# Kernel optimization log

Measured on AMD Instinct MI355X. Metric: run time of the kernel, lower is better.

## Reference

```python
import jax, jax.numpy as jnp
import numpy as np

N = 4096      # tokens per modality
DIM = 514     # input feature dim
OUT = 256     # out_dim (per-head width, head=1)
NC = 2        # num_classes
LN_EPS = 1e-5


def setup_inputs() -> dict:
    key = jax.random.key(0)
    ks = jax.random.split(key, 12)
    def nrm(k, shape, s=0.02):
        return jax.random.normal(k, shape, dtype=jnp.float32) * s
    return {
        "t1": jax.random.normal(ks[0], (N, DIM), dtype=jnp.float32),
        "t2": jax.random.normal(ks[1], (N, DIM), dtype=jnp.float32),
        "t1c": jax.random.normal(ks[2], (N, DIM), dtype=jnp.float32),
        "Wqkv1": nrm(ks[3], (DIM, 3 * OUT)), "bqkv1": jnp.zeros((3 * OUT,), jnp.float32),
        "Wqkv2": nrm(ks[4], (DIM, 3 * OUT)), "bqkv2": jnp.zeros((3 * OUT,), jnp.float32),
        "Wqkv3": nrm(ks[5], (DIM, 3 * OUT)), "bqkv3": jnp.zeros((3 * OUT,), jnp.float32),
        "Wo1": nrm(ks[6], (2 * OUT, DIM)), "bo1": jnp.zeros((DIM,), jnp.float32),
        "Wo2": nrm(ks[7], (2 * OUT, DIM)), "bo2": jnp.zeros((DIM,), jnp.float32),
        "Wo3": nrm(ks[8], (2 * OUT, DIM)), "bo3": jnp.zeros((DIM,), jnp.float32),
        "ln_g": jnp.ones((3 * DIM,), jnp.float32),
        "ln_b": jnp.zeros((3 * DIM,), jnp.float32),
        "Wh": nrm(ks[9], (3 * DIM, NC)), "bh": jnp.zeros((NC,), jnp.float32),
    }


def _forward(t1, t2, t1c, Wqkv1, bqkv1, Wqkv2, bqkv2, Wqkv3, bqkv3,
             Wo1, bo1, Wo2, bo2, Wo3, bo3, ln_g, ln_b, Wh, bh):
    # QKV projections (head=1 so no head reshape needed)
    q1, k1, v1 = jnp.split(t1 @ Wqkv1 + bqkv1, 3, axis=-1)   # each [n, OUT]
    q2, k2, v2 = jnp.split(t2 @ Wqkv2 + bqkv2, 3, axis=-1)
    q3, k3, v3 = jnp.split(t1c @ Wqkv3 + bqkv3, 3, axis=-1)

    # Six cross-attention instances batched into one group dim g=6.
    # Order: out12, out13, out21, out23, out31, out32  (q_x attends to k_y/v_y)
    qs = jnp.stack([q2, q3, q1, q3, q1, q2])                  # [6, n, OUT]
    ks_ = jnp.stack([k1, k1, k2, k2, k3, k3])
    vs = jnp.stack([v1, v1, v2, v2, v3, v3])
    # NOTE: original code applies NO 1/sqrt(d) scale
    attn = jax.nn.softmax(jnp.einsum('gid,gjd->gij', qs, ks_), axis=-1)
    outs = jnp.einsum('gij,gjd->gid', attn, vs)               # [6, n, OUT]
    out12, out13, out21, out23, out31, out32 = outs

    # residual add with duplicated keys, then per-modality output proj + residual
    t1r = jnp.concatenate([out21, out31], -1) + jnp.concatenate([k1, k1], -1)
    t2r = jnp.concatenate([out12, out32], -1) + jnp.concatenate([k2, k2], -1)
    t3r = jnp.concatenate([out13, out23], -1) + jnp.concatenate([k3, k3], -1)
    a1 = t1r @ Wo1 + bo1 + t1                                 # [n, DIM]
    a2 = t2r @ Wo2 + bo2 + t2
    a3 = t3r @ Wo3 + bo3 + t1c

    atten = jnp.concatenate([a1, a2, a3], -1)                 # [n, 3*DIM]
    mu = jnp.mean(atten, axis=-1, keepdims=True)
    var = jnp.var(atten, axis=-1, keepdims=True)
    normed = (atten - mu) * jax.lax.rsqrt(var + LN_EPS) * ln_g + ln_b
    out = normed @ Wh + bh                                    # [n, NC]
    feat = atten[None]                                        # [1, n, 3*DIM]
    return out, feat


def reference(t1, t2, t1c, Wqkv1, bqkv1, Wqkv2, bqkv2, Wqkv3, bqkv3,
              Wo1, bo1, Wo2, bo2, Wo3, bo3, ln_g, ln_b, Wh, bh):
    return _forward(t1, t2, t1c, Wqkv1, bqkv1, Wqkv2, bqkv2, Wqkv3, bqkv3,
                    Wo1, bo1, Wo2, bo2, Wo3, bo3, ln_g, ln_b, Wh, bh)
```

## Files before the change

kernel.cpp:

```cpp
#include <hip/hip_runtime.h>
#include <hip/hip_bf16.h>

typedef unsigned short u16;
typedef unsigned int u32;
typedef __attribute__((ext_vector_type(8))) __bf16 bf16x8;
typedef __attribute__((ext_vector_type(4))) float f32x4;
typedef __attribute__((ext_vector_type(16))) float f32x16;

#define N_TOK 4096
#define DIMF  514
#define KPAD  544
#define OUT3  768
#define OUTD  256
#define RDIM  512
#define FDIM  1542
#define SHIFT 16.0f
#define NCHUNK 4
#define KTILES ((N_TOK / NCHUNK) / 32)

__device__ __forceinline__ bf16x8 ld_frag(const u16* p) {
    return __builtin_bit_cast(bf16x8, *reinterpret_cast<const uint4*>(p));
}
__device__ __forceinline__ u16 f2bf(float x) {
    return __builtin_bit_cast(u16, __float2bfloat16(x));
}
__device__ __forceinline__ float bf2f(u16 u) {
    return __bfloat162float(__builtin_bit_cast(__hip_bfloat16, u));
}
__device__ __forceinline__ f32x16 mfma_b(bf16x8 a, bf16x8 b, f32x16 c) {
    return __builtin_amdgcn_mfma_f32_32x32x16_bf16(a, b, c, 0, 0, 0);
}
__device__ __forceinline__ f32x4 mfma16(bf16x8 a, bf16x8 b, f32x4 c) {
    return __builtin_amdgcn_mfma_f32_16x16x32_bf16(a, b, c, 0, 0, 0);
}
__device__ __forceinline__ void gl_lds16(const u16* g, u16* l) {
    __builtin_amdgcn_global_load_lds(
        (const __attribute__((address_space(1))) void*)(g),
        (__attribute__((address_space(3))) void*)(l), 16, 0, 0);
}

__global__ void prep_kernel(const float* __restrict__ t1, const float* __restrict__ t2,
                            const float* __restrict__ t1c,
                            const float* __restrict__ W1, const float* __restrict__ W2,
                            const float* __restrict__ W3,
                            const float* __restrict__ Wo1, const float* __restrict__ Wo2,
                            const float* __restrict__ Wo3,
                            u16* __restrict__ tA, u16* __restrict__ WqkvT,
                            u16* __restrict__ WoT)
{
    int idx = blockIdx.x * blockDim.x + threadIdx.x;
    const int TA_N = 3 * N_TOK * KPAD;
    const int WQ_N = 3 * OUT3 * KPAD;
    const int WO_N = 3 * DIMF * RDIM;
    if (idx < TA_N) {
        int m = idx / (N_TOK * KPAD);
        int rem = idx - m * (N_TOK * KPAD);
        int row = rem / KPAD;
        int col = rem - row * KPAD;
        const float* t = (m == 0) ? t1 : (m == 1) ? t2 : t1c;
        tA[idx] = (col < DIMF) ? f2bf(t[row * DIMF + col]) : (u16)0;
    } else if (idx < TA_N + WQ_N) {
        int i = idx - TA_N;
        int m = i / (OUT3 * KPAD);
        int rem = i - m * (OUT3 * KPAD);
        int n = rem / KPAD;
        int c = rem - n * KPAD;
        const float* W = (m == 0) ? W1 : (m == 1) ? W2 : W3;
        WqkvT[i] = (c < DIMF) ? f2bf(W[c * OUT3 + n]) : (u16)0;
    } else if (idx < TA_N + WQ_N + WO_N) {
        int i = idx - TA_N - WQ_N;
        int m = i / (DIMF * RDIM);
        int rem = i - m * (DIMF * RDIM);
        int n = rem / RDIM;
        int c = rem - n * RDIM;
        const float* W = (m == 0) ? Wo1 : (m == 1) ? Wo2 : Wo3;
        WoT[i] = f2bf(W[c * DIMF + n]);
    }
}

__global__ __launch_bounds__(256, 1) void qkv_gemm(
    const u16* __restrict__ tA, const u16* __restrict__ WqkvT,
    const float* __restrict__ b1, const float* __restrict__ b2, const float* __restrict__ b3,
    u16* __restrict__ qbuf, u16* __restrict__ kbuf, u16* __restrict__ vT)
{
    const int mt = blockIdx.x, nt = blockIdx.y, mod = blockIdx.z;
    const u16* A = tA + mod * (N_TOK * KPAD);
    const u16* B = WqkvT + mod * (OUT3 * KPAD);
    const float* bias = (mod == 0) ? b1 : (mod == 1) ? b2 : b3;

    __shared__ alignas(16) u16 Al[128 * 40];
    __shared__ alignas(16) u16 Bl[128 * 40];

    const int tid = threadIdx.x;
    const int lane = tid & 63;
    const int w = tid >> 6;
    const int wm = w & 1, wn = w >> 1;
    const int l31 = lane & 31, h = lane >> 5;

    f32x16 acc[2][2];
#pragma unroll
    for (int i = 0; i < 2; i++)
#pragma unroll
        for (int j = 0; j < 2; j++)
#pragma unroll
            for (int r = 0; r < 16; r++) acc[i][j][r] = 0.f;

    for (int kt = 0; kt < KPAD / 32; kt++) {
#pragma unroll
        for (int it = 0; it < 2; it++) {
            int idx = it * 256 + tid;
            int row = idx >> 2;
            int c8 = (idx & 3) * 8;
            uint4 va = *reinterpret_cast<const uint4*>(&A[(mt * 128 + row) * KPAD + kt * 32 + c8]);
            *reinterpret_cast<uint4*>(&Al[row * 40 + c8]) = va;
            uint4 vb = *reinterpret_cast<const uint4*>(&B[(nt * 128 + row) * KPAD + kt * 32 + c8]);
            *reinterpret_cast<uint4*>(&Bl[row * 40 + c8]) = vb;
        }
        __syncthreads();
#pragma unroll
        for (int kc = 0; kc < 2; kc++) {
            bf16x8 af[2], bfr[2];
#pragma unroll
            for (int mr = 0; mr < 2; mr++)
                af[mr] = ld_frag(&Al[(wm * 64 + mr * 32 + l31) * 40 + kc * 16 + h * 8]);
#pragma unroll
            for (int nr = 0; nr < 2; nr++)
                bfr[nr] = ld_frag(&Bl[(wn * 64 + nr * 32 + l31) * 40 + kc * 16 + h * 8]);
#pragma unroll
            for (int mr = 0; mr < 2; mr++)
#pragma unroll
                for (int nr = 0; nr < 2; nr++)
                    acc[mr][nr] = mfma_b(af[mr], bfr[nr], acc[mr][nr]);
        }
        __syncthreads();
    }

    u16* qb = qbuf + mod * (N_TOK * OUTD);
    u16* kb = kbuf + mod * (N_TOK * OUTD);
    u16* vb = vT + mod * (OUTD * N_TOK);
#pragma unroll
    for (int mr = 0; mr < 2; mr++)
#pragma unroll
        for (int nr = 0; nr < 2; nr++)
#pragma unroll
            for (int r = 0; r < 16; r++) {
                int row = mt * 128 + wm * 64 + mr * 32 + (r & 3) + 8 * (r >> 2) + 4 * h;
                int col = nt * 128 + wn * 64 + nr * 32 + l31;
                u16 bv = f2bf(acc[mr][nr][r] + bias[col]);
                int cs = col >> 8, cc = col & 255;
                if (cs == 0)      qb[row * OUTD + cc] = bv;
                else if (cs == 1) kb[row * OUTD + cc] = bv;
                else              vb[cc * N_TOK + row] = bv;
            }
}

__global__ __launch_bounds__(256, 2) void attn_kernel(
    const u16* __restrict__ qbuf, const u16* __restrict__ kbuf,
    const u16* __restrict__ vT, u16* __restrict__ Opart, float* __restrict__ lpart)
{
    const int qt = blockIdx.x;
    const int g  = blockIdx.y;
    const int c  = blockIdx.z;
    const int kv = g >> 1;
    const int mn = (kv == 0) ? 1 : 0;
    const int mx = (kv == 2) ? 1 : 2;
    const int qm = (g & 1) ? mx : mn;

    const u16* Qg = qbuf + qm * (N_TOK * OUTD);
    const u16* Kg = kbuf + kv * (N_TOK * OUTD);
    const u16* Vg = vT + kv * (OUTD * N_TOK);
    u16* Op = Opart + ((size_t)(c * 6 + g) * N_TOK + qt * 128) * OUTD;
    float* lp = lpart + (c * 6 + g) * N_TOK + qt * 128;

    __shared__ alignas(16) u16 Fbuf[2][32 * 512];

    const int tid = threadIdx.x;
    const int lane = tid & 63;
    const int w = tid >> 6;
    const int l31 = lane & 31, h = lane >> 5;
    const int sl = lane & 15, sg = lane >> 4;
    const int q0 = qt * 128 + w * 32;

    auto stage = [&](int k0, u16* dst) {
        if (w < 2) {
#pragma unroll
            for (int fi = 0; fi < 8; fi++) {
                gl_lds16(&Kg[(k0 + w * 16 + sl) * OUTD + fi * 32 + sg * 8],
                         dst + (w * 8 + fi) * 512);
            }
        } else {
#pragma unroll
            for (int fi = 0; fi < 8; fi++) {
                int f = (w - 2) * 8 + fi;
                int nb = f >> 1, half = f & 1;
                gl_lds16(&Vg[(nb * 32 + l31) * N_TOK + k0 + half * 16 + h * 8],
                         dst + (16 + f) * 512);
            }
        }
    };

    const int k0base = c * (N_TOK / NCHUNK);

    stage(k0base, Fbuf[0]);

    bf16x8 qf[16];
#pragma unroll
    for (int j = 0; j < 8; j++)
#pragma unroll
        for (int qh = 0; qh < 2; qh++)
            qf[2 * j + qh] = ld_frag(&Qg[(q0 + qh * 16 + sl) * OUTD + j * 32 + sg * 8]);

    f32x16 Oacc[8];
#pragma unroll
    for (int nb = 0; nb < 8; nb++)
#pragma unroll
        for (int r = 0; r < 16; r++) Oacc[nb][r] = 0.f;
    float lsA0 = 0.f, lsA1 = 0.f;

    __syncthreads();

    for (int kt = 0; kt < KTILES; kt++) {
        const int p = kt & 1;
        if (kt + 1 < KTILES) stage(k0base + (kt + 1) * 32, Fbuf[p ^ 1]);
        const u16* FB = Fbuf[p];

        f32x4 Sq[2][2];
#pragma unroll
        for (int a = 0; a < 2; a++)
#pragma unroll
            for (int b = 0; b < 2; b++)
#pragma unroll
                for (int r = 0; r < 4; r++) Sq[a][b][r] = 0.f;
        __builtin_amdgcn_s_setprio(1);
#pragma unroll
        for (int j = 0; j < 8; j++) {
            bf16x8 kf0 = ld_frag(&FB[j * 512 + lane * 8]);
            bf16x8 kf1 = ld_frag(&FB[(8 + j) * 512 + lane * 8]);
            Sq[0][0] = mfma16(kf0, qf[2 * j], Sq[0][0]);
            Sq[0][1] = mfma16(kf0, qf[2 * j + 1], Sq[0][1]);
            Sq[1][0] = mfma16(kf1, qf[2 * j], Sq[1][0]);
            Sq[1][1] = mfma16(kf1, qf[2 * j + 1], Sq[1][1]);
        }
        __builtin_amdgcn_s_setprio(0);

        u32 pk[2][2][2];
#pragma unroll
        for (int kh = 0; kh < 2; kh++)
#pragma unroll
            for (int qh = 0; qh < 2; qh++) {
                float e0 = __expf(Sq[kh][qh][0] - SHIFT);
                float e1 = __expf(Sq[kh][qh][1] - SHIFT);
                float e2 = __expf(Sq[kh][qh][2] - SHIFT);
                float e3 = __expf(Sq[kh][qh][3] - SHIFT);
                if (qh == 0) lsA0 += (e0 + e1) + (e2 + e3);
                else         lsA1 += (e0 + e1) + (e2 + e3);
                pk[qh][kh][0] = (u32)f2bf(e0) | ((u32)f2bf(e1) << 16);
                pk[qh][kh][1] = (u32)f2bf(e2) | ((u32)f2bf(e3) << 16);
            }

        asm volatile("v_permlane16_swap_b32 %0, %1" : "+v"(pk[0][0][0]), "+v"(pk[1][0][0]));
        asm volatile("v_permlane16_swap_b32 %0, %1" : "+v"(pk[0][0][1]), "+v"(pk[1][0][1]));
        asm volatile("v_permlane16_swap_b32 %0, %1" : "+v"(pk[0][1][0]), "+v"(pk[1][1][0]));
        asm volatile("v_permlane16_swap_b32 %0, %1" : "+v"(pk[0][1][1]), "+v"(pk[1][1][1]));
        uint4 b0, b1;
        b0.x = pk[0][0][0]; b0.y = pk[0][0][1]; b0.z = pk[1][0][0]; b0.w = pk[1][0][1];
        b1.x = pk[0][1][0]; b1.y = pk[0][1][1]; b1.z = pk[1][1][0]; b1.w = pk[1][1][1];
        bf16x8 pb0 = __builtin_bit_cast(bf16x8, b0);
        bf16x8 pb1 = __builtin_bit_cast(bf16x8, b1);

        __builtin_amdgcn_s_setprio(1);
#pragma unroll
        for (int nb = 0; nb < 8; nb++) {
            bf16x8 vf0 = ld_frag(&FB[(16 + 2 * nb) * 512 + lane * 8]);
            bf16x8 vf1 = ld_frag(&FB[(17 + 2 * nb) * 512 + lane * 8]);
            Oacc[nb] = mfma_b(vf0, pb0, Oacc[nb]);
            Oacc[nb] = mfma_b(vf1, pb1, Oacc[nb]);
        }
        __builtin_amdgcn_s_setprio(0);
        __syncthreads();
    }

    lsA0 += __shfl_xor(lsA0, 16, 64);
    lsA0 += __shfl_xor(lsA0, 32, 64);
    lsA1 += __shfl_xor(lsA1, 16, 64);
    lsA1 += __shfl_xor(lsA1, 32, 64);
    if (lane < 16)      lp[w * 32 + lane] = lsA0;
    else if (lane < 32) lp[w * 32 + lane] = lsA1;

    float* Tb = reinterpret_cast<float*>(&Fbuf[0][0]) + w * (32 * 33);
#pragma unroll
    for (int nb = 0; nb < 8; nb++) {
#pragma unroll
        for (int r = 0; r < 16; r++)
            Tb[((r & 3) + 8 * (r >> 2) + 4 * h) * 33 + l31] = Oacc[nb][r];
        __builtin_amdgcn_s_waitcnt(0);
#pragma unroll
        for (int qq = 0; qq < 16; qq++) {
            float v = Tb[l31 * 33 + qq * 2 + h];
            Op[(w * 32 + qq * 2 + h) * OUTD + nb * 32 + l31] = f2bf(v);
        }
        __builtin_amdgcn_s_waitcnt(0);
    }
}

__global__ __launch_bounds__(256, 1) void combine_kernel(
    const u16* __restrict__ Opart, const float* __restrict__ lpart,
    const u16* __restrict__ kbuf, u16* __restrict__ rbuf)
{
    const int q = blockIdx.x;
    const int g = blockIdx.y;
    const int d = threadIdx.x;
    const int kv = g >> 1;
    const int mn = (kv == 0) ? 1 : 0;
    const int mx = (kv == 2) ? 1 : 2;
    const int qm = (g & 1) ? mx : mn;
    const int sm = (qm == 0) ? 1 : 0;
    const int slot = (kv == sm) ? 0 : 1;

    float o = 0.f, l = 0.f;
#pragma unroll
    for (int c = 0; c < NCHUNK; c++) {
        o += bf2f(Opart[((size_t)(c * 6 + g) * N_TOK + q) * OUTD + d]);
        l += lpart[(c * 6 + g) * N_TOK + q];
    }
    float res = o / l + bf2f(kbuf[qm * (N_TOK * OUTD) + q * OUTD + d]);
    rbuf[qm * (size_t)(N_TOK * RDIM) + q * RDIM + slot * OUTD + d] = f2bf(res);
}

__global__ __launch_bounds__(256, 1) void proj_gemm(
    const u16* __restrict__ rbuf, const u16* __restrict__ WoT,
    const float* __restrict__ bo1, const float* __restrict__ bo2, const float* __restrict__ bo3,
    const float* __restrict__ t1, const float* __restrict__ t2, const float* __restrict__ t1c,
    float* __restrict__ feat)
{
    const int mt = blockIdx.x, nt = blockIdx.y, mod = blockIdx.z;
    const u16* A = rbuf + mod * (N_TOK * RDIM);
    const u16* B = WoT + mod * (DIMF * RDIM);
    const float* bias = (mod == 0) ? bo1 : (mod == 1) ? bo2 : bo3;
    const float* tres = (mod == 0) ? t1 : (mod == 1) ? t2 : t1c;

    __shared__ alignas(16) u16 Al[128 * 40];
    __shared__ alignas(16) u16 Bl[128 * 40];

    const int tid = threadIdx.x;
    const int lane = tid & 63;
    const int w = tid >> 6;
    const int wm = w & 1, wn = w >> 1;
    const int l31 = lane & 31, h = lane >> 5;

    f32x16 acc[2][2];
#pragma unroll
    for (int i = 0; i < 2; i++)
#pragma unroll
        for (int j = 0; j < 2; j++)
#pragma unroll
            for (int r = 0; r < 16; r++) acc[i][j][r] = 0.f;

    for (int kt = 0; kt < RDIM / 32; kt++) {
#pragma unroll
        for (int it = 0; it < 2; it++) {
            int idx = it * 256 + tid;
            int row = idx >> 2;
            int c8 = (idx & 3) * 8;
            uint4 va = *reinterpret_cast<const uint4*>(&A[(mt * 128 + row) * RDIM + kt * 32 + c8]);
            *reinterpret_cast<uint4*>(&Al[row * 40 + c8]) = va;
            int n = nt * 128 + row;
            uint4 vb;
            if (n < DIMF) vb = *reinterpret_cast<const uint4*>(&B[n * RDIM + kt * 32 + c8]);
            else { vb.x = vb.y = vb.z = vb.w = 0u; }
            *reinterpret_cast<uint4*>(&Bl[row * 40 + c8]) = vb;
        }
        __syncthreads();
#pragma unroll
        for (int kc = 0; kc < 2; kc++) {
            bf16x8 af[2], bfr[2];
#pragma unroll
            for (int mr = 0; mr < 2; mr++)
                af[mr] = ld_frag(&Al[(wm * 64 + mr * 32 + l31) * 40 + kc * 16 + h * 8]);
#pragma unroll
            for (int nr = 0; nr < 2; nr++)
                bfr[nr] = ld_frag(&Bl[(wn * 64 + nr * 32 + l31) * 40 + kc * 16 + h * 8]);
#pragma unroll
            for (int mr = 0; mr < 2; mr++)
#pragma unroll
                for (int nr = 0; nr < 2; nr++)
                    acc[mr][nr] = mfma_b(af[mr], bfr[nr], acc[mr][nr]);
        }
        __syncthreads();
    }

#pragma unroll
    for (int mr = 0; mr < 2; mr++)
#pragma unroll
        for (int nr = 0; nr < 2; nr++)
#pragma unroll
            for (int r = 0; r < 16; r++) {
                int row = mt * 128 + wm * 64 + mr * 32 + (r & 3) + 8 * (r >> 2) + 4 * h;
                int col = nt * 128 + wn * 64 + nr * 32 + l31;
                if (col < DIMF) {
                    float v = acc[mr][nr][r] + bias[col] + tres[row * DIMF + col];
                    feat[row * FDIM + mod * DIMF + col] = v;
                }
            }
}

__global__ __launch_bounds__(256, 1) void ln_head(
    const float* __restrict__ feat, const float* __restrict__ gam,
    const float* __restrict__ bet, const float* __restrict__ Wh,
    const float* __restrict__ bh, float* __restrict__ out)
{
    const int row = blockIdx.x;
    const float* x = feat + row * FDIM;
    const int tid = threadIdx.x;
    float v[7];
    float s = 0.f, ss = 0.f;
#pragma unroll
    for (int i = 0; i < 7; i++) {
        int idx = tid + i * 256;
        float val = (idx < FDIM) ? x[idx] : 0.f;
        v[i] = val; s += val; ss += val * val;
    }
#pragma unroll
    for (int m = 1; m < 64; m <<= 1) { s += __shfl_xor(s, m, 64); ss += __shfl_xor(ss, m, 64); }
    __shared__ float red[8];
    const int w = tid >> 6, lane = tid & 63;
    if (lane == 0) { red[w] = s; red[4 + w] = ss; }
    __syncthreads();
    s = red[0] + red[1] + red[2] + red[3];
    ss = red[4] + red[5] + red[6] + red[7];
    const float mu = s / (float)FDIM;
    const float var = ss / (float)FDIM - mu * mu;
    const float rstd = rsqrtf(var + 1e-5f);
    float a0 = 0.f, a1 = 0.f;
#pragma unroll
    for (int i = 0; i < 7; i++) {
        int idx = tid + i * 256;
        if (idx < FDIM) {
            float nv = (v[i] - mu) * rstd * gam[idx] + bet[idx];
            a0 += nv * Wh[idx * 2];
            a1 += nv * Wh[idx * 2 + 1];
        }
    }
#pragma unroll
    for (int m = 1; m < 64; m <<= 1) { a0 += __shfl_xor(a0, m, 64); a1 += __shfl_xor(a1, m, 64); }
    __shared__ float red2[8];
    if (lane == 0) { red2[w] = a0; red2[4 + w] = a1; }
    __syncthreads();
    if (tid == 0) {
        out[row * 2 + 0] = red2[0] + red2[1] + red2[2] + red2[3] + bh[0];
        out[row * 2 + 1] = red2[4] + red2[5] + red2[6] + red2[7] + bh[1];
    }
}

extern "C" void kernel_launch(void* const* d_in, const int* in_sizes, int n_in,
                              void* d_out, int out_size, void* d_ws, size_t ws_size,
                              hipStream_t stream)
{
    const float* t1    = (const float*)d_in[0];
    const float* t2    = (const float*)d_in[1];
    const float* t1c   = (const float*)d_in[2];
    const float* Wqkv1 = (const float*)d_in[3];
    const float* bqkv1 = (const float*)d_in[4];
    const float* Wqkv2 = (const float*)d_in[5];
    const float* bqkv2 = (const float*)d_in[6];
    const float* Wqkv3 = (const float*)d_in[7];
    const float* bqkv3 = (const float*)d_in[8];
    const float* Wo1   = (const float*)d_in[9];
    const float* bo1   = (const float*)d_in[10];
    const float* Wo2   = (const float*)d_in[11];
    const float* bo2   = (const float*)d_in[12];
    const float* Wo3   = (const float*)d_in[13];
    const float* bo3   = (const float*)d_in[14];
    const float* ln_g  = (const float*)d_in[15];
    const float* ln_b  = (const float*)d_in[16];
    const float* Wh    = (const float*)d_in[17];
    const float* bh    = (const float*)d_in[18];

    char* ws = (char*)d_ws;
    size_t off = 0;
    u16* tA    = (u16*)(ws + off); off += (size_t)3 * N_TOK * KPAD * 2;
    u16* WqkvT = (u16*)(ws + off); off += (size_t)3 * OUT3 * KPAD * 2;
    u16* WoT   = (u16*)(ws + off); off += (size_t)3 * DIMF * RDIM * 2;
    u16* qbuf  = (u16*)(ws + off); off += (size_t)3 * N_TOK * OUTD * 2;
    u16* kbuf  = (u16*)(ws + off); off += (size_t)3 * N_TOK * OUTD * 2;
    u16* vT    = (u16*)(ws + off); off += (size_t)3 * OUTD * N_TOK * 2;
    u16* rbuf  = (u16*)(ws + off); off += (size_t)3 * N_TOK * RDIM * 2;
    u16* Opart = (u16*)(ws + off); off += (size_t)NCHUNK * 6 * N_TOK * OUTD * 2;
    float* lpart = (float*)(ws + off); off += (size_t)NCHUNK * 6 * N_TOK * 4;

    float* out  = (float*)d_out;
    float* feat = out + N_TOK * 2;

    const int prep_total = 3 * N_TOK * KPAD + 3 * OUT3 * KPAD + 3 * DIMF * RDIM;
    prep_kernel<<<(prep_total + 255) / 256, 256, 0, stream>>>(
        t1, t2, t1c, Wqkv1, Wqkv2, Wqkv3, Wo1, Wo2, Wo3, tA, WqkvT, WoT);

    qkv_gemm<<<dim3(32, 6, 3), 256, 0, stream>>>(
        tA, WqkvT, bqkv1, bqkv2, bqkv3, qbuf, kbuf, vT);

    attn_kernel<<<dim3(32, 6, NCHUNK), 256, 0, stream>>>(qbuf, kbuf, vT, Opart, lpart);

    combine_kernel<<<dim3(N_TOK, 6), 256, 0, stream>>>(Opart, lpart, kbuf, rbuf);

    proj_gemm<<<dim3(32, 5, 3), 256, 0, stream>>>(
        rbuf, WoT, bo1, bo2, bo3, t1, t2, t1c, feat);

    ln_head<<<4096, 256, 0, stream>>>(feat, ln_g, ln_b, Wh, bh, out);
}
```

Measured before the change: 325.6 us.

## Double-buffer GEMM tiles via direct global-to-LDS loads in fragment order

Both the QKV and output-projection GEMMs now stage A/B tiles with global_load_lds directly into LDS. The LDS layout is arranged in MFMA fragment order and double-buffered, so the next k-tile loads while the current one is computed. The projection weight is zero-padded to 640 rows so the bounds check on B loads goes away, and launch bounds allow two blocks per CU. This trades a bit more LDS and padding memory for less register staging and better load/compute overlap.

After: 330.7 us. About the same (+1.5%).

```diff
diff --git a/kernel.cpp b/kernel.cpp
--- a/kernel.cpp
+++ b/kernel.cpp
@@ -13,6 +13,7 @@
 #define OUT3  768
 #define OUTD  256
 #define RDIM  512
+#define DIMP  640
 #define FDIM  1542
 #define SHIFT 16.0f
 #define NCHUNK 4
@@ -51,7 +52,7 @@
     int idx = blockIdx.x * blockDim.x + threadIdx.x;
     const int TA_N = 3 * N_TOK * KPAD;
     const int WQ_N = 3 * OUT3 * KPAD;
-    const int WO_N = 3 * DIMF * RDIM;
+    const int WO_N = 3 * DIMP * RDIM;
     if (idx < TA_N) {
         int m = idx / (N_TOK * KPAD);
         int rem = idx - m * (N_TOK * KPAD);
@@ -69,16 +70,16 @@
         WqkvT[i] = (c < DIMF) ? f2bf(W[c * OUT3 + n]) : (u16)0;
     } else if (idx < TA_N + WQ_N + WO_N) {
         int i = idx - TA_N - WQ_N;
-        int m = i / (DIMF * RDIM);
-        int rem = i - m * (DIMF * RDIM);
+        int m = i / (DIMP * RDIM);
+        int rem = i - m * (DIMP * RDIM);
         int n = rem / RDIM;
         int c = rem - n * RDIM;
         const float* W = (m == 0) ? Wo1 : (m == 1) ? Wo2 : Wo3;
-        WoT[i] = f2bf(W[c * DIMF + n]);
-    }
-}
-
-__global__ __launch_bounds__(256, 1) void qkv_gemm(
+        WoT[i] = (n < DIMF) ? f2bf(W[c * DIMF + n]) : (u16)0;
+    }
+}
+
+__global__ __launch_bounds__(256, 2) void qkv_gemm(
     const u16* __restrict__ tA, const u16* __restrict__ WqkvT,
     const float* __restrict__ b1, const float* __restrict__ b2, const float* __restrict__ b3,
     u16* __restrict__ qbuf, u16* __restrict__ kbuf, u16* __restrict__ vT)
@@ -88,8 +89,7 @@
     const u16* B = WqkvT + mod * (OUT3 * KPAD);
     const float* bias = (mod == 0) ? b1 : (mod == 1) ? b2 : b3;
 
-    __shared__ alignas(16) u16 Al[128 * 40];
-    __shared__ alignas(16) u16 Bl[128 * 40];
+    __shared__ alignas(16) u16 Fbuf[2][16 * 512];
 
     const int tid = threadIdx.x;
     const int lane = tid & 63;
@@ -97,6 +97,18 @@
     const int wm = w & 1, wn = w >> 1;
     const int l31 = lane & 31, h = lane >> 5;
 
+    auto stage = [&](int kt, u16* dst) {
+#pragma unroll
+        for (int fi = 0; fi < 4; fi++) {
+            int f = w * 4 + fi;
+            int rb = (f & 7) >> 1, kc = f & 1;
+            const u16* src = (f < 8)
+                ? &A[(mt * 128 + rb * 32 + l31) * KPAD + kt * 32 + kc * 16 + h * 8]
+                : &B[(nt * 128 + rb * 32 + l31) * KPAD + kt * 32 + kc * 16 + h * 8];
+            gl_lds16(src, dst + f * 512);
+        }
+    };
+
     f32x16 acc[2][2];
 #pragma unroll
     for (int i = 0; i < 2; i++)
@@ -105,27 +117,22 @@
 #pragma unroll
             for (int r = 0; r < 16; r++) acc[i][j][r] = 0.f;
 
+    stage(0, Fbuf[0]);
+    __syncthreads();
+
     for (int kt = 0; kt < KPAD / 32; kt++) {
-#pragma unroll
-        for (int it = 0; it < 2; it++) {
-            int idx = it * 256 + tid;
-            int row = idx >> 2;
-            int c8 = (idx & 3) * 8;
-            uint4 va = *reinterpret_cast<const uint4*>(&A[(mt * 128 + row) * KPAD + kt * 32 + c8]);
-            *reinterpret_cast<uint4*>(&Al[row * 40 + c8]) = va;
-            uint4 vb = *reinterpret_cast<const uint4*>(&B[(nt * 128 + row) * KPAD + kt * 32 + c8]);
-            *reinterpret_cast<uint4*>(&Bl[row * 40 + c8]) = vb;
-        }
-        __syncthreads();
+        const int p = kt & 1;
+        if (kt + 1 < KPAD / 32) stage(kt + 1, Fbuf[p ^ 1]);
+        const u16* FB = Fbuf[p];
 #pragma unroll
         for (int kc = 0; kc < 2; kc++) {
             bf16x8 af[2], bfr[2];
 #pragma unroll
             for (int mr = 0; mr < 2; mr++)
-                af[mr] = ld_frag(&Al[(wm * 64 + mr * 32 + l31) * 40 + kc * 16 + h * 8]);
+                af[mr] = ld_frag(&FB[((wm * 2 + mr) * 2 + kc) * 512 + lane * 8]);
 #pragma unroll
             for (int nr = 0; nr < 2; nr++)
-                bfr[nr] = ld_frag(&Bl[(wn * 64 + nr * 32 + l31) * 40 + kc * 16 + h * 8]);
+                bfr[nr] = ld_frag(&FB[(8 + (wn * 2 + nr) * 2 + kc) * 512 + lane * 8]);
 #pragma unroll
             for (int mr = 0; mr < 2; mr++)
 #pragma unroll
@@ -327,7 +334,7 @@
     rbuf[qm * (size_t)(N_TOK * RDIM) + q * RDIM + slot * OUTD + d] = f2bf(res);
 }
 
-__global__ __launch_bounds__(256, 1) void proj_gemm(
+__global__ __launch_bounds__(256, 2) void proj_gemm(
     const u16* __restrict__ rbuf, const u16* __restrict__ WoT,
     const float* __restrict__ bo1, const float* __restrict__ bo2, const float* __restrict__ bo3,
     const float* __restrict__ t1, const float* __restrict__ t2, const float* __restrict__ t1c,
@@ -335,12 +342,11 @@
 {
     const int mt = blockIdx.x, nt = blockIdx.y, mod = blockIdx.z;
     const u16* A = rbuf + mod * (N_TOK * RDIM);
-    const u16* B = WoT + mod * (DIMF * RDIM);
+    const u16* B = WoT + mod * (DIMP * RDIM);
     const float* bias = (mod == 0) ? bo1 : (mod == 1) ? bo2 : bo3;
     const float* tres = (mod == 0) ? t1 : (mod == 1) ? t2 : t1c;
 
-    __shared__ alignas(16) u16 Al[128 * 40];
-    __shared__ alignas(16) u16 Bl[128 * 40];
+    __shared__ alignas(16) u16 Fbuf[2][16 * 512];
 
     const int tid = threadIdx.x;
     const int lane = tid & 63;
@@ -348,6 +354,18 @@
     const int wm = w & 1, wn = w >> 1;
     const int l31 = lane & 31, h = lane >> 5;
 
+    auto stage = [&](int kt, u16* dst) {
+#pragma unroll
+        for (int fi = 0; fi < 4; fi++) {
+            int f = w * 4 + fi;
+            int rb = (f & 7) >> 1, kc = f & 1;
+            const u16* src = (f < 8)
+                ? &A[(mt * 128 + rb * 32 + l31) * RDIM + kt * 32 + kc * 16 + h * 8]
+                : &B[(nt * 128 + rb * 32 + l31) * RDIM + kt * 32 + kc * 16 + h * 8];
+            gl_lds16(src, dst + f * 512);
+        }
+    };
+
     f32x16 acc[2][2];
 #pragma unroll
     for (int i = 0; i < 2; i++)
@@ -356,30 +374,22 @@
 #pragma unroll
             for (int r = 0; r < 16; r++) acc[i][j][r] = 0.f;
 
+    stage(0, Fbuf[0]);
+    __syncthreads();
+
     for (int kt = 0; kt < RDIM / 32; kt++) {
-#pragma unroll
-        for (int it = 0; it < 2; it++) {
-            int idx = it * 256 + tid;
-            int row = idx >> 2;
-            int c8 = (idx & 3) * 8;
-            uint4 va = *reinterpret_cast<const uint4*>(&A[(mt * 128 + row) * RDIM + kt * 32 + c8]);
-            *reinterpret_cast<uint4*>(&Al[row * 40 + c8]) = va;
-            int n = nt * 128 + row;
-            uint4 vb;
-            if (n < DIMF) vb = *reinterpret_cast<const uint4*>(&B[n * RDIM + kt * 32 + c8]);
-            else { vb.x = vb.y = vb.z = vb.w = 0u; }
-            *reinterpret_cast<uint4*>(&Bl[row * 40 + c8]) = vb;
-        }
-        __syncthreads();
+        const int p = kt & 1;
+        if (kt + 1 < RDIM / 32) stage(kt + 1, Fbuf[p ^ 1]);
+        const u16* FB = Fbuf[p];
 #pragma unroll
         for (int kc = 0; kc < 2; kc++) {
             bf16x8 af[2], bfr[2];
 #pragma unroll
             for (int mr = 0; mr < 2; mr++)
-                af[mr] = ld_frag(&Al[(wm * 64 + mr * 32 + l31) * 40 + kc * 16 + h * 8]);
+                af[mr] = ld_frag(&FB[((wm * 2 + mr) * 2 + kc) * 512 + lane * 8]);
 #pragma unroll
             for (int nr = 0; nr < 2; nr++)
-                bfr[nr] = ld_frag(&Bl[(wn * 64 + nr * 32 + l31) * 40 + kc * 16 + h * 8]);
+                bfr[nr] = ld_frag(&FB[(8 + (wn * 2 + nr) * 2 + kc) * 512 + lane * 8]);
 #pragma unroll
             for (int mr = 0; mr < 2; mr++)
 #pragma unroll
@@ -480,7 +490,7 @@
     size_t off = 0;
     u16* tA    = (u16*)(ws + off); off += (size_t)3 * N_TOK * KPAD * 2;
     u16* WqkvT = (u16*)(ws + off); off += (size_t)3 * OUT3 * KPAD * 2;
-    u16* WoT   = (u16*)(ws + off); off += (size_t)3 * DIMF * RDIM * 2;
+    u16* WoT   = (u16*)(ws + off); off += (size_t)3 * DIMP * RDIM * 2;
     u16* qbuf  = (u16*)(ws + off); off += (size_t)3 * N_TOK * OUTD * 2;
     u16* kbuf  = (u16*)(ws + off); off += (size_t)3 * N_TOK * OUTD * 2;
     u16* vT    = (u16*)(ws + off); off += (size_t)3 * OUTD * N_TOK * 2;
@@ -491,7 +501,7 @@
     float* out  = (float*)d_out;
     float* feat = out + N_TOK * 2;
 
-    const int prep_total = 3 * N_TOK * KPAD + 3 * OUT3 * KPAD + 3 * DIMF * RDIM;
+    const int prep_total = 3 * N_TOK * KPAD + 3 * OUT3 * KPAD + 3 * DIMP * RDIM;
     prep_kernel<<<(prep_total + 255) / 256, 256, 0, stream>>>(
         t1, t2, t1c, Wqkv1, Wqkv2, Wqkv3, Wo1, Wo2, Wo3, tA, WqkvT, WoT);
 
```
